# Performance work log

Hardware: AMD Instinct MI355X
Metric: run time of the kernel (lower is better)

## Reference

```python
import jax, jax.numpy as jnp
import numpy as np

B, IN, H, Z = 2048, 1024, 1024, 256


def setup_inputs() -> dict:
    key = jax.random.key(0)
    ks = jax.random.split(key, 17)
    s = 1.0 / np.sqrt(H)  # matches reset_parameters uniform(-stdv, stdv)
    u = lambda k, shape: jax.random.uniform(k, shape, minval=-s, maxval=s, dtype=jnp.float32)
    return {
        'src_x': jax.random.normal(ks[0], (B, IN), dtype=jnp.float32),
        'h': jax.random.normal(ks[1], (B, H), dtype=jnp.float32),
        'c': jax.random.normal(ks[2], (B, H), dtype=jnp.float32),
        'src_meta': jax.random.normal(ks[3], (B, Z), dtype=jnp.float32),
        'zh_w': u(ks[4], (4 * Z, Z)),
        'zh_b': u(ks[5], (4 * Z,)),
        'zx_w': u(ks[6], (4 * Z, Z)),
        'zx_b': u(ks[7], (4 * Z,)),
        'zb_w': u(ks[8], (4 * Z, Z)),
        'dh_w': u(ks[9], (4, H, Z)),
        'dx_w': u(ks[10], (4, H, Z)),
        'db_w': u(ks[11], (4, H, Z)),
        'db_b': u(ks[12], (4, H)),
        'w_h': u(ks[13], (4, H, H)),
        'w_x': u(ks[14], (4, H, IN)),
        'ln_w': u(ks[15], (4, H)),
        'ln_b': u(ks[16], (4, H)),
    }


def reference(src_x, h, c, src_meta, zh_w, zh_b, zx_w, zx_b, zb_w,
              dh_w, dx_w, db_w, db_b, w_h, w_x, ln_w, ln_b):
    b = src_x.shape[0]
    # hypernetwork projections, reshaped to [B, 4 gates, Z]
    zh = (src_meta @ zh_w.T + zh_b).reshape(b, 4, -1)
    zx = (src_meta @ zx_w.T + zx_b).reshape(b, 4, -1)
    zb = (src_meta @ zb_w.T).reshape(b, 4, -1)
    # per-gate scaling vectors d_h, d_x and bias d_b: [B, 4, H]
    d_h = jnp.einsum('bgz,ghz->bgh', zh, dh_w)
    d_x = jnp.einsum('bgz,ghz->bgh', zx, dx_w)
    d_b = jnp.einsum('bgz,ghz->bgh', zb, db_w) + db_b[None]
    # main LSTM matmuls: [B, 4, H]
    wh = jnp.einsum('ghj,bj->bgh', w_h, h)
    wx = jnp.einsum('ghj,bj->bgh', w_x, src_x)
    y = d_h * wh + d_x * wx + d_b
    # per-gate LayerNorm over hidden dim (eps = 1e-5, torch default)
    mu = jnp.mean(y, axis=-1, keepdims=True)
    var = jnp.var(y, axis=-1, keepdims=True)
    yn = (y - mu) * jax.lax.rsqrt(var + 1e-5) * ln_w[None] + ln_b[None]
    i, f, g, o = yn[:, 0], yn[:, 1], yn[:, 2], yn[:, 3]
    c_next = jax.nn.sigmoid(f) * c + jax.nn.sigmoid(i) * jnp.tanh(g)
    h_next = jax.nn.sigmoid(o) * jnp.tanh(c_next)
    return (h_next, c_next)
```

## Files before the change

kernel.cpp:

```cpp
#include <hip/hip_runtime.h>

typedef __attribute__((ext_vector_type(4))) float f32x4;
typedef __attribute__((ext_vector_type(8))) short bf16x8;

#define DEVFN static __device__ __forceinline__

DEVFN unsigned short f2bf(float f) {
  union { float f; unsigned u; } x; x.f = f;
  unsigned r = x.u + 0x7fffu + ((x.u >> 16) & 1u);
  return (unsigned short)(r >> 16);
}
DEVFN float bf2f(unsigned short u) {
  union { unsigned u; float f; } x; x.u = ((unsigned)u) << 16;
  return x.f;
}

DEVFN void gload_lds16(const unsigned short* g, unsigned short* l) {
  __builtin_amdgcn_global_load_lds(
      (const __attribute__((address_space(1))) unsigned int*)g,
      (__attribute__((address_space(3))) unsigned int*)l, 16, 0, 0);
}

#define NSEG 8
struct SegTable {
  const float* src[NSEG];
  unsigned short* dst[NSEG];
  int chunks[NSEG];
};

__global__ __launch_bounds__(256) void prep_kernel(
    SegTable st, int castChunks,
    const float* __restrict__ zh_w, const float* __restrict__ zx_w,
    const float* __restrict__ zb_w, unsigned short* __restrict__ WzT,
    const float* __restrict__ zh_b, const float* __restrict__ zx_b,
    const float* __restrict__ db_b, const float* __restrict__ dh_w,
    const float* __restrict__ dx_w, float* __restrict__ F) {
  __shared__ float T[64][65];
  const int tid = threadIdx.x;
  int b = blockIdx.x;

  if (b < castChunks) {
    int c = b, s = 0;
    while (c >= st.chunks[s]) { c -= st.chunks[s]; ++s; }
    const float* src = st.src[s] + (long)c * 4096;
    unsigned short* dst = st.dst[s] + (long)c * 4096;
#pragma unroll
    for (int i = 0; i < 4; ++i) {
      float4 v = *(const float4*)(src + tid * 4 + i * 1024);
      ushort4 o;
      o.x = f2bf(v.x); o.y = f2bf(v.y); o.z = f2bf(v.z); o.w = f2bf(v.w);
      *(ushort4*)(dst + tid * 4 + i * 1024) = o;
    }
    return;
  }
  b -= castChunks;

  if (b < 192) {
    const int zz = b >> 4, rem = b & 15;
    const int t = zz >> 2, g = zz & 3;
    const float* src =
        (t == 0 ? zh_w : (t == 1 ? zx_w : zb_w)) + (long)g * 65536;
    unsigned short* dst = WzT + (long)zz * 65536;
    const int j0 = (rem & 3) * 64, k0 = (rem >> 2) * 64;
    const int jr = tid >> 2, kc = (tid & 3) * 16;
#pragma unroll
    for (int i = 0; i < 4; ++i) {
      float4 v = *(const float4*)(src + (long)(j0 + jr) * 256 + k0 + kc + i * 4);
      T[jr][kc + i * 4 + 0] = v.x;
      T[jr][kc + i * 4 + 1] = v.y;
      T[jr][kc + i * 4 + 2] = v.z;
      T[jr][kc + i * 4 + 3] = v.w;
    }
    __syncthreads();
    const int kr = tid >> 2, jc = (tid & 3) * 16;
    unsigned short tmp[16];
#pragma unroll
    for (int i = 0; i < 16; ++i) tmp[i] = f2bf(T[jc + i][kr]);
    *(bf16x8*)(dst + (long)(k0 + kr) * 256 + j0 + jc) = *(bf16x8*)&tmp[0];
    *(bf16x8*)(dst + (long)(k0 + kr) * 256 + j0 + jc + 8) = *(bf16x8*)&tmp[8];
    return;
  }
  b -= 192;

  if (b >= 128) {
    const int idx = (b - 128) * 1024 + tid * 4;
    *(float4*)(F + 8192 + idx) = *(const float4*)(db_b + idx);
    return;
  }
  const int wgid = b * 4 + (tid >> 6);
  const int lane = tid & 63;
  const int t = wgid >> 8, g = (wgid >> 6) & 3, hbase = (wgid & 63) * 16;
  const float* zb = (t == 0 ? zh_b : zx_b) + g * 256;
  const float* dw = (t == 0 ? dh_w : dx_w) + (long)g * 262144;
  float4 zv = *(const float4*)(zb + lane * 4);
#pragma unroll
  for (int i = 0; i < 16; ++i) {
    const int h = hbase + i;
    float4 wv = *(const float4*)(dw + (long)h * 256 + lane * 4);
    float s = zv.x * wv.x + zv.y * wv.y + zv.z * wv.z + zv.w * wv.w;
#pragma unroll
    for (int off = 32; off; off >>= 1) s += __shfl_down(s, off);
    if (lane == 0) F[(t * 4 + g) * 1024 + h] = s;
  }
}

DEVFN void gemm128_body(const unsigned short* __restrict__ A,
                        const unsigned short* __restrict__ W,
                        unsigned short* __restrict__ C,
                        const float* __restrict__ bias,
                        int lda, int ldb, int ldc, int K,
                        int bx, int by,
                        unsigned short* As, unsigned short* Bs) {
  const int m0 = by * 128, n0 = bx * 128;
  const int tid = threadIdx.x;
  const int lane = tid & 63, wid = tid >> 6;
  const int wr = wid >> 1, wc = wid & 1;

  const int srow = tid >> 2, scol = (tid & 3) * 8;
  const unsigned short* Ag0 = A + (long)(m0 + srow) * lda + scol;
  const unsigned short* Ag1 = A + (long)(m0 + 64 + srow) * lda + scol;
  const unsigned short* Wg0 = W + (long)(n0 + srow) * ldb + scol;
  const unsigned short* Wg1 = W + (long)(n0 + 64 + srow) * ldb + scol;
  unsigned short* As0 = &As[tid * 8];
  unsigned short* As1 = &As[2048 + tid * 8];
  unsigned short* Bs0 = &Bs[tid * 8];
  unsigned short* Bs1 = &Bs[2048 + tid * 8];

  const int r = lane & 15, q = lane >> 4;

  f32x4 acc[4][4];
#pragma unroll
  for (int m = 0; m < 4; ++m)
#pragma unroll
    for (int n = 0; n < 4; ++n) acc[m][n] = (f32x4)0.f;

  for (int k0 = 0; k0 < K; k0 += 32) {
    gload_lds16(Ag0 + k0, As0);
    gload_lds16(Ag1 + k0, As1);
    gload_lds16(Wg0 + k0, Bs0);
    gload_lds16(Wg1 + k0, Bs1);
    __syncthreads();

    bf16x8 af[4], bfr[4];
#pragma unroll
    for (int m = 0; m < 4; ++m)
      af[m] = *(const bf16x8*)&As[(wr * 64 + m * 16 + r) * 32 + q * 8];
#pragma unroll
    for (int n = 0; n < 4; ++n)
      bfr[n] = *(const bf16x8*)&Bs[(wc * 64 + n * 16 + r) * 32 + q * 8];
#pragma unroll
    for (int m = 0; m < 4; ++m)
#pragma unroll
      for (int n = 0; n < 4; ++n)
        acc[m][n] = __builtin_amdgcn_mfma_f32_16x16x32_bf16(af[m], bfr[n],
                                                            acc[m][n], 0, 0, 0);
    __syncthreads();
  }

#pragma unroll
  for (int m = 0; m < 4; ++m) {
    const int row = m0 + wr * 64 + m * 16 + q * 4;
#pragma unroll
    for (int n = 0; n < 4; ++n) {
      const int col = n0 + wc * 64 + n * 16 + r;
      float bv = bias ? bias[col] : 0.f;
#pragma unroll
      for (int j = 0; j < 4; ++j) {
        float v = acc[m][n][j] + bv;
        C[(long)(row + j) * ldc + col] = f2bf(v);
      }
    }
  }
}

__global__ __launch_bounds__(256) void gemm_e(
    const unsigned short* __restrict__ Wd, const unsigned short* __restrict__ WzT,
    unsigned short* __restrict__ E) {
  __shared__ __align__(16) unsigned short As[4096];
  __shared__ __align__(16) unsigned short Bs[4096];
  const int zz = blockIdx.z;
  gemm128_body(Wd + (long)zz * 262144, WzT + (long)zz * 65536,
               E + (long)zz * 262144, nullptr,
               256, 256, 256, 256, blockIdx.x, blockIdx.y, As, Bs);
}

__global__ __launch_bounds__(256) void gemm_d(
    const unsigned short* __restrict__ meta_bf, const unsigned short* __restrict__ E,
    unsigned short* __restrict__ dall, const float* __restrict__ F) {
  __shared__ __align__(16) unsigned short As[4096];
  __shared__ __align__(16) unsigned short Bs[4096];
  const int zz = blockIdx.z;
  unsigned short* C = dall + (long)(zz >> 2) * 8388608 + (zz & 3) * 1024;
  gemm128_body(meta_bf, E + (long)zz * 262144, C, F + zz * 1024,
               256, 256, 4096, 256, blockIdx.x, blockIdx.y, As, Bs);
}

__global__ __launch_bounds__(512, 2) void gemm256_whx(
    const unsigned short* __restrict__ Aall,
    const unsigned short* __restrict__ Ball,
    unsigned short* __restrict__ Call) {
  __shared__ __align__(16) unsigned short As[2][2][8192];
  __shared__ __align__(16) unsigned short Bs[2][2][8192];

  const int bid = blockIdx.x;
  const int swz = (bid & 7) * 32 + (bid >> 3);
  const int z = swz >> 7;
  const int rr = swz & 127;
  const int sb = rr >> 5, wq = rr & 31;
  const int my = (sb & 1) * 4 + (wq >> 3);
  const int nx = (sb >> 1) * 8 + (wq & 7);

  const unsigned short* Ag = Aall + (long)z * 2097152 + (long)my * 262144;
  const unsigned short* Bg = Ball + (long)z * 4194304 + (long)nx * 262144;
  unsigned short* Cg = Call + (long)z * 8388608 + (long)my * 1048576 + nx * 256;

  const int tid = threadIdx.x;
  const int lane = tid & 63, wid = tid >> 6;
  const int wm = wid >> 2, wn = wid & 3;
  const int fr = lane & 15, fq = lane >> 4;
  const int s0 = fq ^ (fr & 7);

  const int srow = tid >> 3, sslot = tid & 7;
  const int gcol = (sslot ^ (srow & 7)) * 8;
  const unsigned short* AgS = Ag + (long)srow * 1024 + gcol;
  const unsigned short* BgS = Bg + (long)srow * 1024 + gcol;

  auto stageA = [&](int buf, int half, int kt) {
    const unsigned short* s = AgS + half * 131072 + kt * 64;
    unsigned short* d = &As[buf][half][tid * 8];
    gload_lds16(s, d);
    gload_lds16(s + 65536, d + 4096);
  };
  auto stageB = [&](int buf, int half, int kt) {
    const unsigned short* s = BgS + half * 131072 + kt * 64;
    unsigned short* d = &Bs[buf][half][tid * 8];
    gload_lds16(s, d);
    gload_lds16(s + 65536, d + 4096);
  };

  int aoff[4], boff[2];
#pragma unroll
  for (int mf = 0; mf < 4; ++mf)
    aoff[mf] = (wm * 64 + mf * 16 + fr) * 64 + s0 * 8;
#pragma unroll
  for (int nf = 0; nf < 2; ++nf)
    boff[nf] = (wn * 32 + nf * 16 + fr) * 64 + s0 * 8;

  f32x4 acc[2][2][4][2];
#pragma unroll
  for (int i = 0; i < 2; ++i)
#pragma unroll
    for (int j = 0; j < 2; ++j)
#pragma unroll
      for (int m = 0; m < 4; ++m)
#pragma unroll
        for (int n = 0; n < 2; ++n) acc[i][j][m][n] = (f32x4)0.f;

  stageA(0, 0, 0); stageA(0, 1, 0); stageB(0, 0, 0); stageB(0, 1, 0);
  stageA(1, 0, 1); stageB(1, 0, 1); stageB(1, 1, 1);
  asm volatile("s_waitcnt vmcnt(6)" ::: "memory");
  __builtin_amdgcn_s_barrier();

  bf16x8 af[4][2], bA[2][2], bB[2][2];

#define PH_SYNC                                          \
  __builtin_amdgcn_s_barrier();                          \
  asm volatile("s_waitcnt lgkmcnt(0)" ::: "memory");     \
  __builtin_amdgcn_sched_barrier(0);

#define PH_MFMA(MH, NH, BR)                              \
  __builtin_amdgcn_s_setprio(1);                         \
  _Pragma("unroll")                                      \
  for (int mf = 0; mf < 4; ++mf)                         \
    _Pragma("unroll")                                    \
    for (int nf = 0; nf < 2; ++nf) {                     \
      acc[MH][NH][mf][nf] = __builtin_amdgcn_mfma_f32_16x16x32_bf16( \
          af[mf][0], BR[nf][0], acc[MH][NH][mf][nf], 0, 0, 0);       \
      acc[MH][NH][mf][nf] = __builtin_amdgcn_mfma_f32_16x16x32_bf16( \
          af[mf][1], BR[nf][1], acc[MH][NH][mf][nf], 0, 0, 0);       \
    }                                                    \
  __builtin_amdgcn_s_setprio(0);

#pragma unroll 2
  for (int T = 0; T < 16; ++T) {
    const int buf = T & 1, nb = buf ^ 1;

    {
      const unsigned short* Ab = &As[buf][0][0];
      const unsigned short* Bb = &Bs[buf][0][0];
#pragma unroll
      for (int mf = 0; mf < 4; ++mf) {
        af[mf][0] = *(const bf16x8*)(Ab + aoff[mf]);
        af[mf][1] = *(const bf16x8*)(Ab + (aoff[mf] ^ 32));
      }
#pragma unroll
      for (int nf = 0; nf < 2; ++nf) {
        bA[nf][0] = *(const bf16x8*)(Bb + boff[nf]);
        bA[nf][1] = *(const bf16x8*)(Bb + (boff[nf] ^ 32));
      }
      if (T < 15) stageA(nb, 1, T + 1);
      PH_SYNC;
      PH_MFMA(0, 0, bA);
      __builtin_amdgcn_s_barrier();
    }
    {
      const unsigned short* Bb = &Bs[buf][1][0];
#pragma unroll
      for (int nf = 0; nf < 2; ++nf) {
        bB[nf][0] = *(const bf16x8*)(Bb + boff[nf]);
        bB[nf][1] = *(const bf16x8*)(Bb + (boff[nf] ^ 32));
      }
      if (T < 14) stageA(buf, 0, T + 2);
      PH_SYNC;
      PH_MFMA(0, 1, bB);
      __builtin_amdgcn_s_barrier();
    }
    {
      const unsigned short* Ab = &As[buf][1][0];
#pragma unroll
      for (int mf = 0; mf < 4; ++mf) {
        af[mf][0] = *(const bf16x8*)(Ab + aoff[mf]);
        af[mf][1] = *(const bf16x8*)(Ab + (aoff[mf] ^ 32));
      }
      if (T < 14) stageB(buf, 0, T + 2);
      PH_SYNC;
      PH_MFMA(1, 0, bA);
      __builtin_amdgcn_s_barrier();
    }
    {
      if (T < 14) stageB(buf, 1, T + 2);
      PH_SYNC;
      PH_MFMA(1, 1, bB);
      if (T < 14) {
        asm volatile("s_waitcnt vmcnt(6)" ::: "memory");
      } else if (T == 14) {
        asm volatile("s_waitcnt vmcnt(0)" ::: "memory");
      }
      __builtin_amdgcn_s_barrier();
    }
  }
#undef PH_SYNC
#undef PH_MFMA

#pragma unroll
  for (int mh = 0; mh < 2; ++mh)
#pragma unroll
    for (int nh = 0; nh < 2; ++nh)
#pragma unroll
      for (int mf = 0; mf < 4; ++mf)
#pragma unroll
        for (int nf = 0; nf < 2; ++nf) {
          const int row = mh * 128 + wm * 64 + mf * 16 + fq * 4;
          const int col = nh * 128 + wn * 32 + nf * 16 + fr;
#pragma unroll
          for (int j = 0; j < 4; ++j)
            Cg[(long)(row + j) * 4096 + col] = f2bf(acc[mh][nh][mf][nf][j]);
        }
}

DEVFN void ld4bf(const unsigned short* p, float* o) {
  ushort4 v = *(const ushort4*)p;
  o[0] = bf2f(v.x); o[1] = bf2f(v.y); o[2] = bf2f(v.z); o[3] = bf2f(v.w);
}

__global__ __launch_bounds__(256) void epilogue_kernel(
    const unsigned short* __restrict__ d_all,
    const unsigned short* __restrict__ whx,
    const float* __restrict__ c_in,
    const float* __restrict__ ln_w, const float* __restrict__ ln_b,
    float* __restrict__ out) {
  const long b = blockIdx.x;
  const int t = threadIdx.x;
  const int lane = t & 63, wid = t >> 6;

  const unsigned short* dh = d_all + b * 4096;
  const unsigned short* dx = d_all + 8388608L + b * 4096;
  const unsigned short* db = d_all + 16777216L + b * 4096;
  const unsigned short* wh = whx + b * 4096;
  const unsigned short* wx = whx + 8388608L + b * 4096;

  __shared__ float redS[4][4], redQ[4][4];
  float y[4][4];

#pragma unroll
  for (int g = 0; g < 4; ++g) {
    const int base = g * 1024 + t * 4;
    float fdh[4], fdx[4], fdb[4], fwh[4], fwx[4];
    ld4bf(dh + base, fdh);
    ld4bf(dx + base, fdx);
    ld4bf(db + base, fdb);
    ld4bf(wh + base, fwh);
    ld4bf(wx + base, fwx);
    float s = 0.f, sq = 0.f;
#pragma unroll
    for (int j = 0; j < 4; ++j) {
      float v = fdh[j] * fwh[j] + fdx[j] * fwx[j] + fdb[j];
      y[g][j] = v;
      s += v;
      sq += v * v;
    }
#pragma unroll
    for (int off = 32; off; off >>= 1) {
      s += __shfl_down(s, off);
      sq += __shfl_down(sq, off);
    }
    if (lane == 0) { redS[g][wid] = s; redQ[g][wid] = sq; }
  }
  __syncthreads();

  float yn[4][4];
#pragma unroll
  for (int g = 0; g < 4; ++g) {
    float S = redS[g][0] + redS[g][1] + redS[g][2] + redS[g][3];
    float SQ = redQ[g][0] + redQ[g][1] + redQ[g][2] + redQ[g][3];
    float mu = S * (1.f / 1024.f);
    float var = SQ * (1.f / 1024.f) - mu * mu;
    float rs = rsqrtf(var + 1e-5f);
    const int base = g * 1024 + t * 4;
    float4 lw = *(const float4*)(ln_w + base);
    float4 lb = *(const float4*)(ln_b + base);
    yn[g][0] = (y[g][0] - mu) * rs * lw.x + lb.x;
    yn[g][1] = (y[g][1] - mu) * rs * lw.y + lb.y;
    yn[g][2] = (y[g][2] - mu) * rs * lw.z + lb.z;
    yn[g][3] = (y[g][3] - mu) * rs * lw.w + lb.w;
  }

  float4 cp = *(const float4*)(c_in + b * 1024 + t * 4);
  float cin[4] = {cp.x, cp.y, cp.z, cp.w};
  float hn[4], cn[4];
#pragma unroll
  for (int j = 0; j < 4; ++j) {
    float ii = yn[0][j], ff = yn[1][j], gg = yn[2][j], oo = yn[3][j];
    float si = 1.f / (1.f + expf(-ii));
    float sf = 1.f / (1.f + expf(-ff));
    float so = 1.f / (1.f + expf(-oo));
    float cnj = sf * cin[j] + si * tanhf(gg);
    cn[j] = cnj;
    hn[j] = so * tanhf(cnj);
  }
  float4 ho = {hn[0], hn[1], hn[2], hn[3]};
  float4 co = {cn[0], cn[1], cn[2], cn[3]};
  *(float4*)(out + b * 1024 + t * 4) = ho;
  *(float4*)(out + 2097152L + b * 1024 + t * 4) = co;
}

extern "C" void kernel_launch(void* const* d_in, const int* in_sizes, int n_in,
                              void* d_out, int out_size, void* d_ws,
                              size_t ws_size, hipStream_t stream) {
  const float* src_x = (const float*)d_in[0];
  const float* h_in  = (const float*)d_in[1];
  const float* c_in  = (const float*)d_in[2];
  const float* meta  = (const float*)d_in[3];
  const float* zh_w  = (const float*)d_in[4];
  const float* zh_b  = (const float*)d_in[5];
  const float* zx_w  = (const float*)d_in[6];
  const float* zx_b  = (const float*)d_in[7];
  const float* zb_w  = (const float*)d_in[8];
  const float* dh_w  = (const float*)d_in[9];
  const float* dx_w  = (const float*)d_in[10];
  const float* db_w  = (const float*)d_in[11];
  const float* db_b  = (const float*)d_in[12];
  const float* w_h   = (const float*)d_in[13];
  const float* w_x   = (const float*)d_in[14];
  const float* ln_w  = (const float*)d_in[15];
  const float* ln_b  = (const float*)d_in[16];

  char* ws = (char*)d_ws;
  unsigned short* h_bf    = (unsigned short*)(ws + 0);
  unsigned short* x_bf    = (unsigned short*)(ws + 4194304);
  unsigned short* meta_bf = (unsigned short*)(ws + 8388608);
  unsigned short* Wh      = (unsigned short*)(ws + 9437184);
  unsigned short* Wx      = (unsigned short*)(ws + 17825792);
  unsigned short* Wd      = (unsigned short*)(ws + 26214400);
  unsigned short* WzT     = (unsigned short*)(ws + 32505856);
  unsigned short* E       = (unsigned short*)(ws + 34078720);
  float*          F       = (float*)(ws + 40370176);
  unsigned short* dall    = (unsigned short*)(ws + 40419328);
  unsigned short* whx     = (unsigned short*)(ws + 90750976);
  if (ws_size < 124305408) return;

  SegTable st;
  int i = 0, total = 0;
  auto add = [&](const float* s, unsigned short* d, int n) {
    st.src[i] = s; st.dst[i] = d; st.chunks[i] = n / 4096;
    total += n / 4096; ++i;
  };
  add(h_in, h_bf, 2048 * 1024);
  add(src_x, x_bf, 2048 * 1024);
  add(meta, meta_bf, 2048 * 256);
  add(w_h, Wh, 4096 * 1024);
  add(w_x, Wx, 4096 * 1024);
  add(dh_w, Wd, 4 * 1024 * 256);
  add(dx_w, Wd + 1048576, 4 * 1024 * 256);
  add(db_w, Wd + 2097152, 4 * 1024 * 256);

  prep_kernel<<<total + 192 + 132, 256, 0, stream>>>(
      st, total, zh_w, zx_w, zb_w, WzT, zh_b, zx_b, db_b, dh_w, dx_w, F);

  gemm_e<<<dim3(2, 8, 12), 256, 0, stream>>>(Wd, WzT, E);

  gemm_d<<<dim3(8, 16, 12), 256, 0, stream>>>(meta_bf, E, dall, F);

  gemm256_whx<<<256, 512, 0, stream>>>(h_bf, Wh, whx);

  epilogue_kernel<<<2048, 256, 0, stream>>>(dall, whx, c_in, ln_w, ln_b,
                                            (float*)d_out);
}
```

Measured before the change: 114.8 us.

## Merge GEMM B-staging phases and widen epilogue to 16-byte loads, two rows per block

In the main GEMM loop, the two B-tile staging steps are merged into one phase, which removes a barrier and a sync point per iteration. The epilogue now handles two batch rows per 256-thread block. Each thread processes 8 elements with 16-byte bf16x8 loads instead of 8-byte loads, and the grid is halved. The aim is fewer barriers and fewer, wider memory transactions, at the cost of more registers per thread and possibly less overlap between issuing loads and running MFMAs.

```diff
diff --git a/kernel.cpp b/kernel.cpp
--- a/kernel.cpp
+++ b/kernel.cpp
@@ -322,14 +322,9 @@
         af[mf][0] = *(const bf16x8*)(Ab + aoff[mf]);
         af[mf][1] = *(const bf16x8*)(Ab + (aoff[mf] ^ 32));
       }
-      if (T < 14) stageB(buf, 0, T + 2);
+      if (T < 14) { stageB(buf, 0, T + 2); stageB(buf, 1, T + 2); }
       PH_SYNC;
       PH_MFMA(1, 0, bA);
-      __builtin_amdgcn_s_barrier();
-    }
-    {
-      if (T < 14) stageB(buf, 1, T + 2);
-      PH_SYNC;
       PH_MFMA(1, 1, bB);
       if (T < 14) {
         asm volatile("s_waitcnt vmcnt(6)" ::: "memory");
@@ -358,20 +353,16 @@
         }
 }
 
-DEVFN void ld4bf(const unsigned short* p, float* o) {
-  ushort4 v = *(const ushort4*)p;
-  o[0] = bf2f(v.x); o[1] = bf2f(v.y); o[2] = bf2f(v.z); o[3] = bf2f(v.w);
-}
-
 __global__ __launch_bounds__(256) void epilogue_kernel(
     const unsigned short* __restrict__ d_all,
     const unsigned short* __restrict__ whx,
     const float* __restrict__ c_in,
     const float* __restrict__ ln_w, const float* __restrict__ ln_b,
     float* __restrict__ out) {
-  const long b = blockIdx.x;
   const int t = threadIdx.x;
-  const int lane = t & 63, wid = t >> 6;
+  const int sub = t >> 7, tt = t & 127;
+  const long b = (long)blockIdx.x * 2 + sub;
+  const int lane = t & 63, wv = (t >> 6) & 1;
 
   const unsigned short* dh = d_all + b * 4096;
   const unsigned short* dx = d_all + 8388608L + b * 4096;
@@ -379,23 +370,24 @@
   const unsigned short* wh = whx + b * 4096;
   const unsigned short* wx = whx + 8388608L + b * 4096;
 
-  __shared__ float redS[4][4], redQ[4][4];
-  float y[4][4];
+  __shared__ float redS[2][4][2], redQ[2][4][2];
+  float y[4][8];
 
 #pragma unroll
   for (int g = 0; g < 4; ++g) {
-    const int base = g * 1024 + t * 4;
-    float fdh[4], fdx[4], fdb[4], fwh[4], fwx[4];
-    ld4bf(dh + base, fdh);
-    ld4bf(dx + base, fdx);
-    ld4bf(db + base, fdb);
-    ld4bf(wh + base, fwh);
-    ld4bf(wx + base, fwx);
+    const int base = g * 1024 + tt * 8;
+    bf16x8 vdh = *(const bf16x8*)(dh + base);
+    bf16x8 vdx = *(const bf16x8*)(dx + base);
+    bf16x8 vdb = *(const bf16x8*)(db + base);
+    bf16x8 vwh = *(const bf16x8*)(wh + base);
+    bf16x8 vwx = *(const bf16x8*)(wx + base);
     float s = 0.f, sq = 0.f;
 #pragma unroll
-    for (int j = 0; j < 4; ++j) {
-      float v = fdh[j] * fwh[j] + fdx[j] * fwx[j] + fdb[j];
-      y[g][j] = v;
+    for (int e = 0; e < 8; ++e) {
+      float v = bf2f((unsigned short)vdh[e]) * bf2f((unsigned short)vwh[e]) +
+                bf2f((unsigned short)vdx[e]) * bf2f((unsigned short)vwx[e]) +
+                bf2f((unsigned short)vdb[e]);
+      y[g][e] = v;
       s += v;
       sq += v * v;
     }
@@ -404,44 +396,50 @@
       s += __shfl_down(s, off);
       sq += __shfl_down(sq, off);
     }
-    if (lane == 0) { redS[g][wid] = s; redQ[g][wid] = sq; }
+    if (lane == 0) { redS[sub][g][wv] = s; redQ[sub][g][wv] = sq; }
   }
   __syncthreads();
 
-  float yn[4][4];
+  float yn[4][8];
 #pragma unroll
   for (int g = 0; g < 4; ++g) {
-    float S = redS[g][0] + redS[g][1] + redS[g][2] + redS[g][3];
-    float SQ = redQ[g][0] + redQ[g][1] + redQ[g][2] + redQ[g][3];
+    float S = redS[sub][g][0] + redS[sub][g][1];
+    float SQ = redQ[sub][g][0] + redQ[sub][g][1];
     float mu = S * (1.f / 1024.f);
     float var = SQ * (1.f / 1024.f) - mu * mu;
     float rs = rsqrtf(var + 1e-5f);
-    const int base = g * 1024 + t * 4;
-    float4 lw = *(const float4*)(ln_w + base);
-    float4 lb = *(const float4*)(ln_b + base);
-    yn[g][0] = (y[g][0] - mu) * rs * lw.x + lb.x;
-    yn[g][1] = (y[g][1] - mu) * rs * lw.y + lb.y;
-    yn[g][2] = (y[g][2] - mu) * rs * lw.z + lb.z;
-    yn[g][3] = (y[g][3] - mu) * rs * lw.w + lb.w;
-  }
-
-  float4 cp = *(const float4*)(c_in + b * 1024 + t * 4);
-  float cin[4] = {cp.x, cp.y, cp.z, cp.w};
-  float hn[4], cn[4];
-#pragma unroll
-  for (int j = 0; j < 4; ++j) {
-    float ii = yn[0][j], ff = yn[1][j], gg = yn[2][j], oo = yn[3][j];
+    const int base = g * 1024 + tt * 8;
+    float4 lw0 = *(const float4*)(ln_w + base);
+    float4 lw1 = *(const float4*)(ln_w + base + 4);
+    float4 lb0 = *(const float4*)(ln_b + base);
+    float4 lb1 = *(const float4*)(ln_b + base + 4);
+    float lw[8] = {lw0.x, lw0.y, lw0.z, lw0.w, lw1.x, lw1.y, lw1.z, lw1.w};
+    float lb[8] = {lb0.x, lb0.y, lb0.z, lb0.w, lb1.x, lb1.y, lb1.z, lb1.w};
+#pragma unroll
+    for (int e = 0; e < 8; ++e)
+      yn[g][e] = (y[g][e] - mu) * rs * lw[e] + lb[e];
+  }
+
+  float4 cp0 = *(const float4*)(c_in + b * 1024 + tt * 8);
+  float4 cp1 = *(const float4*)(c_in + b * 1024 + tt * 8 + 4);
+  float cin[8] = {cp0.x, cp0.y, cp0.z, cp0.w, cp1.x, cp1.y, cp1.z, cp1.w};
+  float hn[8], cn[8];
+#pragma unroll
+  for (int e = 0; e < 8; ++e) {
+    float ii = yn[0][e], ff = yn[1][e], gg = yn[2][e], oo = yn[3][e];
     float si = 1.f / (1.f + expf(-ii));
     float sf = 1.f / (1.f + expf(-ff));
     float so = 1.f / (1.f + expf(-oo));
-    float cnj = sf * cin[j] + si * tanhf(gg);
-    cn[j] = cnj;
-    hn[j] = so * tanhf(cnj);
-  }
-  float4 ho = {hn[0], hn[1], hn[2], hn[3]};
-  float4 co = {cn[0], cn[1], cn[2], cn[3]};
-  *(float4*)(out + b * 1024 + t * 4) = ho;
-  *(float4*)(out + 2097152L + b * 1024 + t * 4) = co;
+    float cnj = sf * cin[e] + si * tanhf(gg);
+    cn[e] = cnj;
+    hn[e] = so * tanhf(cnj);
+  }
+  float* ho = out + b * 1024 + tt * 8;
+  float* co = out + 2097152L + b * 1024 + tt * 8;
+  *(float4*)(ho) = {hn[0], hn[1], hn[2], hn[3]};
+  *(float4*)(ho + 4) = {hn[4], hn[5], hn[6], hn[7]};
+  *(float4*)(co) = {cn[0], cn[1], cn[2], cn[3]};
+  *(float4*)(co + 4) = {cn[4], cn[5], cn[6], cn[7]};
 }
 
 extern "C" void kernel_launch(void* const* d_in, const int* in_sizes, int n_in,
@@ -503,6 +501,6 @@
 
   gemm256_whx<<<256, 512, 0, stream>>>(h_bf, Wh, whx);
 
-  epilogue_kernel<<<2048, 256, 0, stream>>>(dall, whx, c_in, ln_w, ln_b,
+  epilogue_kernel<<<1024, 256, 0, stream>>>(dall, whx, c_in, ln_w, ln_b,
                                             (float*)d_out);
 }
```

After: 116.9 us. Within noise of the previous version (+1.8%).

## Fuse d-vector GEMM with gating combine into single y kernel

Applied to the files above, without the earlier changes.

Replaces the gemm_d kernel, which wrote three bf16 d_h/d_x/d_b tensors to global memory, with a gemm_y64 kernel. It computes each d tile in LDS and immediately combines it with the wh/wx results, writing only the combined pre-norm y. The epilogue then reads a single tensor instead of five, which cuts global traffic and workspace. Separately, the whx main loop merges two pipeline phases, issuing both B stages together and dropping one barrier per iteration. The trade-off is extra serialization in the new fused kernel (three sequential small GEMMs per block) and a more aggressive issue order in the main GEMM.

```diff
diff --git a/kernel.cpp b/kernel.cpp
--- a/kernel.cpp
+++ b/kernel.cpp
@@ -184,15 +184,115 @@
                256, 256, 256, 256, blockIdx.x, blockIdx.y, As, Bs);
 }
 
-__global__ __launch_bounds__(256) void gemm_d(
-    const unsigned short* __restrict__ meta_bf, const unsigned short* __restrict__ E,
-    unsigned short* __restrict__ dall, const float* __restrict__ F) {
-  __shared__ __align__(16) unsigned short As[4096];
-  __shared__ __align__(16) unsigned short Bs[4096];
-  const int zz = blockIdx.z;
-  unsigned short* C = dall + (long)(zz >> 2) * 8388608 + (zz & 3) * 1024;
-  gemm128_body(meta_bf, E + (long)zz * 262144, C, F + zz * 1024,
-               256, 256, 4096, 256, blockIdx.x, blockIdx.y, As, Bs);
+__global__ __launch_bounds__(256) void gemm_y64(
+    const unsigned short* __restrict__ meta_bf,
+    const unsigned short* __restrict__ E,
+    const unsigned short* __restrict__ whx,
+    const float* __restrict__ F,
+    unsigned short* __restrict__ Y) {
+  __shared__ __align__(16) unsigned short S[8192];
+
+  const int g = blockIdx.z;
+  const int m0 = blockIdx.y * 64, n0 = blockIdx.x * 128;
+  const int tid = threadIdx.x;
+  const int lane = tid & 63, wid = tid >> 6;
+  const int wr = wid >> 1, wc = wid & 1;
+  const int r = lane & 15, q = lane >> 4;
+  const int srow = tid >> 2, scol = (tid & 3) * 8;
+  const int lrow = tid >> 4, lcol = (tid & 15) * 8;
+
+  const unsigned short* Ag0 = meta_bf + (long)(m0 + srow) * 256 + scol;
+  unsigned short* As0 = &S[tid * 8];
+  unsigned short* Bs0 = &S[2048 + tid * 8];
+  unsigned short* Bs1 = &S[4096 + tid * 8];
+
+  float yacc[4][8];
+#pragma unroll
+  for (int i = 0; i < 4; ++i)
+#pragma unroll
+    for (int e = 0; e < 8; ++e) yacc[i][e] = 0.f;
+
+#pragma unroll 1
+  for (int t = 0; t < 3; ++t) {
+    const int zz = t * 4 + g;
+    const unsigned short* W = E + (long)zz * 262144;
+    const unsigned short* Wg0 = W + (long)(n0 + srow) * 256 + scol;
+    const unsigned short* Wg1 = Wg0 + 16384;
+
+    f32x4 acc[2][4];
+#pragma unroll
+    for (int m = 0; m < 2; ++m)
+#pragma unroll
+      for (int n = 0; n < 4; ++n) acc[m][n] = (f32x4)0.f;
+
+    for (int k0 = 0; k0 < 256; k0 += 32) {
+      gload_lds16(Ag0 + k0, As0);
+      gload_lds16(Wg0 + k0, Bs0);
+      gload_lds16(Wg1 + k0, Bs1);
+      __syncthreads();
+
+      bf16x8 af[2], bfr[4];
+#pragma unroll
+      for (int m = 0; m < 2; ++m)
+        af[m] = *(const bf16x8*)&S[(wr * 32 + m * 16 + r) * 32 + q * 8];
+#pragma unroll
+      for (int n = 0; n < 4; ++n)
+        bfr[n] = *(const bf16x8*)&S[2048 + (wc * 64 + n * 16 + r) * 32 + q * 8];
+#pragma unroll
+      for (int m = 0; m < 2; ++m)
+#pragma unroll
+        for (int n = 0; n < 4; ++n)
+          acc[m][n] = __builtin_amdgcn_mfma_f32_16x16x32_bf16(
+              af[m], bfr[n], acc[m][n], 0, 0, 0);
+      __syncthreads();
+    }
+
+    const float* Fz = F + (long)zz * 1024 + n0;
+#pragma unroll
+    for (int n = 0; n < 4; ++n) {
+      const int col = wc * 64 + n * 16 + r;
+      const float fv = Fz[col];
+#pragma unroll
+      for (int m = 0; m < 2; ++m) {
+        const int rowb = wr * 32 + m * 16 + q * 4;
+#pragma unroll
+        for (int j = 0; j < 4; ++j)
+          S[(rowb + j) * 128 + col] = f2bf(acc[m][n][j] + fv);
+      }
+    }
+    __syncthreads();
+
+    if (t < 2) {
+      const unsigned short* wsrc =
+          whx + (long)t * 8388608 + (long)m0 * 4096 + g * 1024 + n0;
+#pragma unroll
+      for (int i = 0; i < 4; ++i) {
+        bf16x8 dv = *(const bf16x8*)&S[(i * 16 + lrow) * 128 + lcol];
+        bf16x8 wv = *(const bf16x8*)(wsrc + (long)(i * 16 + lrow) * 4096 + lcol);
+#pragma unroll
+        for (int e = 0; e < 8; ++e)
+          yacc[i][e] += bf2f((unsigned short)dv[e]) * bf2f((unsigned short)wv[e]);
+      }
+    } else {
+#pragma unroll
+      for (int i = 0; i < 4; ++i) {
+        bf16x8 dv = *(const bf16x8*)&S[(i * 16 + lrow) * 128 + lcol];
+#pragma unroll
+        for (int e = 0; e < 8; ++e)
+          yacc[i][e] += bf2f((unsigned short)dv[e]);
+      }
+    }
+    __syncthreads();
+  }
+
+  unsigned short* Yt = Y + (long)m0 * 4096 + g * 1024 + n0;
+#pragma unroll
+  for (int i = 0; i < 4; ++i) {
+    unsigned short tmp[8];
+#pragma unroll
+    for (int e = 0; e < 8; ++e) tmp[e] = f2bf(yacc[i][e]);
+    *(bf16x8*)(Yt + (long)(i * 16 + lrow) * 4096 + lcol) = *(bf16x8*)&tmp[0];
+  }
 }
 
 __global__ __launch_bounds__(512, 2) void gemm256_whx(
@@ -322,14 +422,9 @@
         af[mf][0] = *(const bf16x8*)(Ab + aoff[mf]);
         af[mf][1] = *(const bf16x8*)(Ab + (aoff[mf] ^ 32));
       }
-      if (T < 14) stageB(buf, 0, T + 2);
+      if (T < 14) { stageB(buf, 0, T + 2); stageB(buf, 1, T + 2); }
       PH_SYNC;
       PH_MFMA(1, 0, bA);
-      __builtin_amdgcn_s_barrier();
-    }
-    {
-      if (T < 14) stageB(buf, 1, T + 2);
-      PH_SYNC;
       PH_MFMA(1, 1, bB);
       if (T < 14) {
         asm volatile("s_waitcnt vmcnt(6)" ::: "memory");
@@ -363,9 +458,8 @@
   o[0] = bf2f(v.x); o[1] = bf2f(v.y); o[2] = bf2f(v.z); o[3] = bf2f(v.w);
 }
 
-__global__ __launch_bounds__(256) void epilogue_kernel(
-    const unsigned short* __restrict__ d_all,
-    const unsigned short* __restrict__ whx,
+__global__ __launch_bounds__(256) void epilogue2(
+    const unsigned short* __restrict__ Y,
     const float* __restrict__ c_in,
     const float* __restrict__ ln_w, const float* __restrict__ ln_b,
     float* __restrict__ out) {
@@ -373,32 +467,15 @@
   const int t = threadIdx.x;
   const int lane = t & 63, wid = t >> 6;
 
-  const unsigned short* dh = d_all + b * 4096;
-  const unsigned short* dx = d_all + 8388608L + b * 4096;
-  const unsigned short* db = d_all + 16777216L + b * 4096;
-  const unsigned short* wh = whx + b * 4096;
-  const unsigned short* wx = whx + 8388608L + b * 4096;
-
   __shared__ float redS[4][4], redQ[4][4];
   float y[4][4];
 
 #pragma unroll
   for (int g = 0; g < 4; ++g) {
-    const int base = g * 1024 + t * 4;
-    float fdh[4], fdx[4], fdb[4], fwh[4], fwx[4];
-    ld4bf(dh + base, fdh);
-    ld4bf(dx + base, fdx);
-    ld4bf(db + base, fdb);
-    ld4bf(wh + base, fwh);
-    ld4bf(wx + base, fwx);
+    ld4bf(Y + b * 4096 + g * 1024 + t * 4, y[g]);
     float s = 0.f, sq = 0.f;
 #pragma unroll
-    for (int j = 0; j < 4; ++j) {
-      float v = fdh[j] * fwh[j] + fdx[j] * fwx[j] + fdb[j];
-      y[g][j] = v;
-      s += v;
-      sq += v * v;
-    }
+    for (int j = 0; j < 4; ++j) { s += y[g][j]; sq += y[g][j] * y[g][j]; }
 #pragma unroll
     for (int off = 32; off; off >>= 1) {
       s += __shfl_down(s, off);
@@ -475,9 +552,9 @@
   unsigned short* WzT     = (unsigned short*)(ws + 32505856);
   unsigned short* E       = (unsigned short*)(ws + 34078720);
   float*          F       = (float*)(ws + 40370176);
-  unsigned short* dall    = (unsigned short*)(ws + 40419328);
-  unsigned short* whx     = (unsigned short*)(ws + 90750976);
-  if (ws_size < 124305408) return;
+  unsigned short* Ybuf    = (unsigned short*)(ws + 40419328);
+  unsigned short* whx     = (unsigned short*)(ws + 57196544);
+  if (ws_size < 90750976) return;
 
   SegTable st;
   int i = 0, total = 0;
@@ -499,10 +576,9 @@
 
   gemm_e<<<dim3(2, 8, 12), 256, 0, stream>>>(Wd, WzT, E);
 
-  gemm_d<<<dim3(8, 16, 12), 256, 0, stream>>>(meta_bf, E, dall, F);
-
   gemm256_whx<<<256, 512, 0, stream>>>(h_bf, Wh, whx);
 
-  epilogue_kernel<<<2048, 256, 0, stream>>>(dall, whx, c_in, ln_w, ln_b,
-                                            (float*)d_out);
-}
+  gemm_y64<<<dim3(8, 32, 4), 256, 0, stream>>>(meta_bf, E, whx, F, Ybuf);
+
+  epilogue2<<<2048, 256, 0, stream>>>(Ybuf, c_in, ln_w, ln_b, (float*)d_out);
+}
```

Result: slower. 119.0 us (+3.7%).

## Replace 128-tile d-projection GEMM with 256-tile pipelined kernel; merge last phases

Applied to the files above, without the earlier changes.

Replaces the 128x128-tile gemm_d, which computes the per-gate d_h/d_x/d_b vectors from meta and E, with a 256x256-tile, 512-thread kernel. The new kernel reuses the double-buffered global_load_lds pipeline from the main Wh/Wx GEMM, with a swizzled block order and the bias added in the epilogue. It also merges the last two MFMA phases in both 256 kernels, staging both B halves at once and dropping one barrier per K step. This aims to raise MFMA reuse and cut LDS barrier overhead. K is only 256, so the deep pipeline has just four iterations, and the grid of 384 large blocks may fill the GPU unevenly.

```diff
diff --git a/kernel.cpp b/kernel.cpp
--- a/kernel.cpp
+++ b/kernel.cpp
@@ -184,15 +184,165 @@
                256, 256, 256, 256, blockIdx.x, blockIdx.y, As, Bs);
 }
 
-__global__ __launch_bounds__(256) void gemm_d(
-    const unsigned short* __restrict__ meta_bf, const unsigned short* __restrict__ E,
-    unsigned short* __restrict__ dall, const float* __restrict__ F) {
-  __shared__ __align__(16) unsigned short As[4096];
-  __shared__ __align__(16) unsigned short Bs[4096];
-  const int zz = blockIdx.z;
-  unsigned short* C = dall + (long)(zz >> 2) * 8388608 + (zz & 3) * 1024;
-  gemm128_body(meta_bf, E + (long)zz * 262144, C, F + zz * 1024,
-               256, 256, 4096, 256, blockIdx.x, blockIdx.y, As, Bs);
+__global__ __launch_bounds__(512, 2) void gemm_d256(
+    const unsigned short* __restrict__ A,
+    const unsigned short* __restrict__ E,
+    unsigned short* __restrict__ dall,
+    const float* __restrict__ F) {
+  __shared__ __align__(16) unsigned short As[2][2][8192];
+  __shared__ __align__(16) unsigned short Bs[2][2][8192];
+
+  const int bid = blockIdx.x;
+  const int swz = (bid & 7) * 48 + (bid >> 3);
+  const int my = swz / 48, nx = swz % 48;
+  const int zz = nx >> 2, hbase = (nx & 3) * 256;
+  const int tt = zz >> 2, g = zz & 3;
+
+  const unsigned short* Ag = A + (long)my * 65536;
+  const unsigned short* Bg = E + (long)nx * 65536;
+  unsigned short* Cg =
+      dall + (long)tt * 8388608 + (long)my * 1048576 + g * 1024 + hbase;
+  const float* Fz = F + zz * 1024 + hbase;
+
+  const int tid = threadIdx.x;
+  const int lane = tid & 63, wid = tid >> 6;
+  const int wm = wid >> 2, wn = wid & 3;
+  const int fr = lane & 15, fq = lane >> 4;
+  const int s0 = fq ^ (fr & 7);
+
+  const int srow = tid >> 3, sslot = tid & 7;
+  const int gcol = (sslot ^ (srow & 7)) * 8;
+  const unsigned short* AgS = Ag + (long)srow * 256 + gcol;
+  const unsigned short* BgS = Bg + (long)srow * 256 + gcol;
+
+  auto stageA = [&](int buf, int half, int kt) {
+    const unsigned short* s = AgS + half * 32768 + kt * 64;
+    unsigned short* d = &As[buf][half][tid * 8];
+    gload_lds16(s, d);
+    gload_lds16(s + 16384, d + 4096);
+  };
+  auto stageB = [&](int buf, int half, int kt) {
+    const unsigned short* s = BgS + half * 32768 + kt * 64;
+    unsigned short* d = &Bs[buf][half][tid * 8];
+    gload_lds16(s, d);
+    gload_lds16(s + 16384, d + 4096);
+  };
+
+  int aoff[4], boff[2];
+#pragma unroll
+  for (int mf = 0; mf < 4; ++mf)
+    aoff[mf] = (wm * 64 + mf * 16 + fr) * 64 + s0 * 8;
+#pragma unroll
+  for (int nf = 0; nf < 2; ++nf)
+    boff[nf] = (wn * 32 + nf * 16 + fr) * 64 + s0 * 8;
+
+  f32x4 acc[2][2][4][2];
+#pragma unroll
+  for (int i = 0; i < 2; ++i)
+#pragma unroll
+    for (int j = 0; j < 2; ++j)
+#pragma unroll
+      for (int m = 0; m < 4; ++m)
+#pragma unroll
+        for (int n = 0; n < 2; ++n) acc[i][j][m][n] = (f32x4)0.f;
+
+  stageA(0, 0, 0); stageA(0, 1, 0); stageB(0, 0, 0); stageB(0, 1, 0);
+  stageA(1, 0, 1); stageB(1, 0, 1); stageB(1, 1, 1);
+  asm volatile("s_waitcnt vmcnt(6)" ::: "memory");
+  __builtin_amdgcn_s_barrier();
+
+  bf16x8 af[4][2], bA[2][2], bB[2][2];
+
+#define PH_SYNC                                          \
+  __builtin_amdgcn_s_barrier();                          \
+  asm volatile("s_waitcnt lgkmcnt(0)" ::: "memory");     \
+  __builtin_amdgcn_sched_barrier(0);
+
+#define PH_MFMA(MH, NH, BR)                              \
+  __builtin_amdgcn_s_setprio(1);                         \
+  _Pragma("unroll")                                      \
+  for (int mf = 0; mf < 4; ++mf)                         \
+    _Pragma("unroll")                                    \
+    for (int nf = 0; nf < 2; ++nf) {                     \
+      acc[MH][NH][mf][nf] = __builtin_amdgcn_mfma_f32_16x16x32_bf16( \
+          af[mf][0], BR[nf][0], acc[MH][NH][mf][nf], 0, 0, 0);       \
+      acc[MH][NH][mf][nf] = __builtin_amdgcn_mfma_f32_16x16x32_bf16( \
+          af[mf][1], BR[nf][1], acc[MH][NH][mf][nf], 0, 0, 0);       \
+    }                                                    \
+  __builtin_amdgcn_s_setprio(0);
+
+#pragma unroll
+  for (int T = 0; T < 4; ++T) {
+    const int buf = T & 1, nb = buf ^ 1;
+
+    {
+      const unsigned short* Ab = &As[buf][0][0];
+      const unsigned short* Bb = &Bs[buf][0][0];
+#pragma unroll
+      for (int mf = 0; mf < 4; ++mf) {
+        af[mf][0] = *(const bf16x8*)(Ab + aoff[mf]);
+        af[mf][1] = *(const bf16x8*)(Ab + (aoff[mf] ^ 32));
+      }
+#pragma unroll
+      for (int nf = 0; nf < 2; ++nf) {
+        bA[nf][0] = *(const bf16x8*)(Bb + boff[nf]);
+        bA[nf][1] = *(const bf16x8*)(Bb + (boff[nf] ^ 32));
+      }
+      if (T < 3) stageA(nb, 1, T + 1);
+      PH_SYNC;
+      PH_MFMA(0, 0, bA);
+      __builtin_amdgcn_s_barrier();
+    }
+    {
+      const unsigned short* Bb = &Bs[buf][1][0];
+#pragma unroll
+      for (int nf = 0; nf < 2; ++nf) {
+        bB[nf][0] = *(const bf16x8*)(Bb + boff[nf]);
+        bB[nf][1] = *(const bf16x8*)(Bb + (boff[nf] ^ 32));
+      }
+      if (T < 2) stageA(buf, 0, T + 2);
+      PH_SYNC;
+      PH_MFMA(0, 1, bB);
+      __builtin_amdgcn_s_barrier();
+    }
+    {
+      const unsigned short* Ab = &As[buf][1][0];
+#pragma unroll
+      for (int mf = 0; mf < 4; ++mf) {
+        af[mf][0] = *(const bf16x8*)(Ab + aoff[mf]);
+        af[mf][1] = *(const bf16x8*)(Ab + (aoff[mf] ^ 32));
+      }
+      if (T < 2) { stageB(buf, 0, T + 2); stageB(buf, 1, T + 2); }
+      PH_SYNC;
+      PH_MFMA(1, 0, bA);
+      PH_MFMA(1, 1, bB);
+      if (T < 2) {
+        asm volatile("s_waitcnt vmcnt(6)" ::: "memory");
+      } else if (T == 2) {
+        asm volatile("s_waitcnt vmcnt(0)" ::: "memory");
+      }
+      __builtin_amdgcn_s_barrier();
+    }
+  }
+#undef PH_SYNC
+#undef PH_MFMA
+
+#pragma unroll
+  for (int mh = 0; mh < 2; ++mh)
+#pragma unroll
+    for (int nh = 0; nh < 2; ++nh)
+#pragma unroll
+      for (int mf = 0; mf < 4; ++mf)
+#pragma unroll
+        for (int nf = 0; nf < 2; ++nf) {
+          const int row = mh * 128 + wm * 64 + mf * 16 + fq * 4;
+          const int col = nh * 128 + wn * 32 + nf * 16 + fr;
+          const float bv = Fz[col];
+#pragma unroll
+          for (int j = 0; j < 4; ++j)
+            Cg[(long)(row + j) * 4096 + col] =
+                f2bf(acc[mh][nh][mf][nf][j] + bv);
+        }
 }
 
 __global__ __launch_bounds__(512, 2) void gemm256_whx(
@@ -322,14 +472,9 @@
         af[mf][0] = *(const bf16x8*)(Ab + aoff[mf]);
         af[mf][1] = *(const bf16x8*)(Ab + (aoff[mf] ^ 32));
       }
-      if (T < 14) stageB(buf, 0, T + 2);
+      if (T < 14) { stageB(buf, 0, T + 2); stageB(buf, 1, T + 2); }
       PH_SYNC;
       PH_MFMA(1, 0, bA);
-      __builtin_amdgcn_s_barrier();
-    }
-    {
-      if (T < 14) stageB(buf, 1, T + 2);
-      PH_SYNC;
       PH_MFMA(1, 1, bB);
       if (T < 14) {
         asm volatile("s_waitcnt vmcnt(6)" ::: "memory");
@@ -499,7 +644,7 @@
 
   gemm_e<<<dim3(2, 8, 12), 256, 0, stream>>>(Wd, WzT, E);
 
-  gemm_d<<<dim3(8, 16, 12), 256, 0, stream>>>(meta_bf, E, dall, F);
+  gemm_d256<<<384, 512, 0, stream>>>(meta_bf, E, dall, F);
 
   gemm256_whx<<<256, 512, 0, stream>>>(h_bf, Wh, whx);
 
```

After: 118.6 us. +3.3%, slower.
